# Optimization experiments

Hardware: AMD Instinct MI355X
Metric: run time of the kernel (lower is better)

## Reference

```python
import jax, jax.numpy as jnp
import numpy as np

N, C, H, W = 4, 15, 320, 320
FEATS_OUT, KSIZE, PAD, CONV_PAD, K_RBF = 32, 11, 11, 5, 31
VMAX = 1.0


def _fft2c(x):
    # fastMRI-style centered orthonormal 2D FFT on complex array [..., H, W]
    x = jnp.fft.ifftshift(x, axes=(-2, -1))
    x = jnp.fft.fft2(x, axes=(-2, -1), norm='ortho')
    return jnp.fft.fftshift(x, axes=(-2, -1))


def _ifft2c(x):
    x = jnp.fft.ifftshift(x, axes=(-2, -1))
    x = jnp.fft.ifft2(x, axes=(-2, -1), norm='ortho')
    return jnp.fft.fftshift(x, axes=(-2, -1))


def _to_c(x):
    return jax.lax.complex(x[..., 0], x[..., 1])


def _to_r(z):
    return jnp.stack([jnp.real(z), jnp.imag(z)], axis=-1)


def setup_inputs() -> dict:
    key = jax.random.key(0)
    ks = jax.random.split(key, 8)
    u_t = jax.random.normal(ks[0], (N, H, W, 2), dtype=jnp.float32)
    f = jax.random.normal(ks[1], (N, C, H, W, 2), dtype=jnp.float32)
    coil_sens = jax.random.normal(ks[2], (N, C, H, W, 2), dtype=jnp.float32)
    sampling_mask = (jax.random.uniform(ks[3], (N, H, W)) < 0.35).astype(jnp.float32)
    conv_kernel = jax.random.normal(ks[4], (FEATS_OUT, 1, KSIZE, KSIZE, 2), dtype=jnp.float32)
    conv_kernel = conv_kernel / np.sqrt(KSIZE * KSIZE * 2 * 1)
    conv_kernel = conv_kernel - jnp.mean(conv_kernel, axis=(1, 2, 3, 4), keepdims=True)
    x0 = jnp.linspace(-VMAX, VMAX, K_RBF, dtype=jnp.float32)
    w = jnp.broadcast_to((0.04 * x0).reshape(1, 1, 1, 1, K_RBF), (1, FEATS_OUT, 1, 1, K_RBF)).astype(jnp.float32)
    mu = x0
    sigma = jnp.array([2.0 * VMAX / (K_RBF - 1)], dtype=jnp.float32)
    lamb = jnp.array([1.0], dtype=jnp.float32)
    return {'u_t': u_t, 'f': f, 'coil_sens': coil_sens, 'sampling_mask': sampling_mask,
            'conv_kernel': conv_kernel, 'w': w, 'mu': mu, 'sigma': sigma, 'lamb': lamb}


def reference(u_t, f, coil_sens, sampling_mask, conv_kernel, w, mu, sigma, lamb):
    dn = ('NCHW', 'OIHW', 'NCHW')
    feats_out = conv_kernel.shape[0]
    k = conv_kernel.shape[2]

    # --- regularizer: reflect-pad, complex conv pair, RBF activation, transposed conv pair ---
    pad_cfg = ((0, 0), (0, 0), (PAD, PAD), (PAD, PAD))
    ur = jnp.pad(u_t[:, None, :, :, 0], pad_cfg, mode='reflect')  # [N,1,Hp,Wp]
    ui = jnp.pad(u_t[:, None, :, :, 1], pad_cfg, mode='reflect')

    def conv(x, Wk):
        return jax.lax.conv_general_dilated(x, Wk, (1, 1), [(CONV_PAD, CONV_PAD)] * 2,
                                            dimension_numbers=dn)

    u_k = conv(ur, conv_kernel[..., 0]) + conv(ui, conv_kernel[..., 1])  # [N,Co,Hp,Wp]

    # RBF activation: sum_i w_i * exp(-(x - mu_i)^2 / (2 sigma^2)), scanned over centers
    wk = jnp.transpose(w[0, :, 0, 0, :])  # [K, Co]
    inv2s2 = 1.0 / (2.0 * sigma[0] ** 2)

    def body(acc, wm):
        wi, mi = wm
        acc = acc + wi[None, :, None, None] * jnp.exp(-jnp.square(u_k - mi) * inv2s2)
        return acc, None

    f_u_k, _ = jax.lax.scan(body, jnp.zeros_like(u_k), (wk, mu))

    # conv_transpose2d(padding=CONV_PAD) == conv with flipped kernel, swapped channels, padding k-1-CONV_PAD
    tpad = k - 1 - CONV_PAD

    def convT(x, Wk):
        Wt = jnp.transpose(Wk[:, :, ::-1, ::-1], (1, 0, 2, 3))  # [I,O,k,k] -> OIHW w/ O=1
        return jax.lax.conv_general_dilated(x, Wt, (1, 1), [(tpad, tpad)] * 2,
                                            dimension_numbers=dn)

    Ru_r = convT(f_u_k, conv_kernel[..., 0])[:, 0]  # [N,Hp,Wp]
    Ru_i = convT(f_u_k, conv_kernel[..., 1])[:, 0]
    Ru = jnp.stack([Ru_r, Ru_i], axis=-1)[:, PAD:-PAD, PAD:-PAD, :] / feats_out  # [N,H,W,2]

    # --- data consistency: A^T (A u - f) (cartesian, os=False) ---
    u_c = _to_c(u_t)              # [N,H,W]
    c_c = _to_c(coil_sens)        # [N,C,H,W]
    f_c = _to_c(f)                # [N,C,H,W]
    m = sampling_mask[:, None]    # [N,1,H,W]
    Au = m * _fft2c(u_c[:, None] * c_c)
    At = jnp.sum(_ifft2c(m * (Au - f_c)) * jnp.conj(c_c), axis=1)  # [N,H,W]
    Du = _to_r(At) * lamb[0]

    return u_t - Ru - Du
```

## Files before the change

kernel.cpp:

```cpp
#include <hip/hip_runtime.h>
#include <hip/hip_bf16.h>
#include <math.h>

#define NN 4
#define CC 15
#define HH 320
#define WW 320
#define HW (HH*WW)
#define FF 32
#define KS 11
#define PADN 11
#define CPAD 5
#define HP 342
#define NK 31
#define NCB (NN*CC)
#define TABN 256

typedef short bf16x8 __attribute__((ext_vector_type(8)));
typedef float f32x4 __attribute__((ext_vector_type(4)));
typedef unsigned short u16x4 __attribute__((ext_vector_type(4)));

#define MFMA16 __builtin_amdgcn_mfma_f32_16x16x32_bf16

__device__ __forceinline__ unsigned int pack_bf(float r, float i) {
  __hip_bfloat16 hr = __float2bfloat16(r), hi = __float2bfloat16(i);
  unsigned short ur = *(unsigned short*)&hr, ui = *(unsigned short*)&hi;
  return (unsigned int)ur | ((unsigned int)ui << 16);
}
__device__ __forceinline__ unsigned short f2b(float x) {
  __hip_bfloat16 h = __float2bfloat16(x);
  return *(unsigned short*)&h;
}
__device__ __forceinline__ float b2f(unsigned short u) {
  __hip_bfloat16 h = *(__hip_bfloat16*)&u;
  return __bfloat162float(h);
}
__device__ __forceinline__ unsigned int rot16(unsigned int x) {
  return (x >> 16) | (x << 16);
}

__global__ void k_dft(unsigned int* __restrict__ Fbf) {
  int idx = blockIdx.x * blockDim.x + threadIdx.x;
  if (idx >= HW) return;
  int k = idx / WW, n = idx % WW;
  int prod = (k - 160) * (n - 160);
  int r = prod % 320; if (r < 0) r += 320;
  float ang = -6.283185307179586f * (float)r / 320.0f;
  const float s = 0.05590169943749474f;
  Fbf[idx] = pack_bf(cosf(ang) * s, sinf(ang) * s);
}

__global__ void k_prep(const float* __restrict__ ck, unsigned int* __restrict__ Wpk) {
  int idx = blockIdx.x * blockDim.x + threadIdx.x;
  if (idx >= 32 * 176) return;
  int o = idx / 176, kw = idx % 176;
  int ky = kw / 16, kx = kw % 16;
  unsigned int v = 0;
  if (kx <= 10) {
    const float* p = &ck[(o * 121 + ky * 11 + kx) * 2];
    v = pack_bf(p[0], p[1]);
  }
  Wpk[idx] = v;
}

__global__ void k_prep2(const float* __restrict__ ck, unsigned short* __restrict__ Wt) {
  int idx = blockIdx.x * blockDim.x + threadIdx.x;
  if (idx >= 2 * 11 * 16 * 32) return;
  int o = idx & 31;
  int ky = (idx >> 5) & 15;
  int rest = idx >> 9;
  int kx = rest % 11, ch = rest / 11;
  unsigned short v = 0;
  if (ky <= 10) v = f2b(ck[(o * 121 + ky * 11 + kx) * 2 + ch]);
  Wt[idx] = v;
}

__global__ void k_rbftab(const float* __restrict__ w, const float* __restrict__ mu,
                         const float* __restrict__ sigma, unsigned short* __restrict__ Tab) {
  int o = blockIdx.x;
  int e = threadIdx.x;
  if (e >= TABN + 1) return;
  float v = -2.0f + (float)e * (4.0f / (float)TABN);
  float sg = sigma[0];
  float nInv = -1.0f / (2.0f * sg * sg);
  float acc = 0.f;
  for (int i = 0; i < NK; i++) {
    float d = v - mu[i];
    acc += w[o * NK + i] * __expf(d * d * nInv);
  }
  Tab[o * 260 + e] = f2b(acc);
}

__global__ __launch_bounds__(256) void k_conv_rbf_mfma(
    const float* __restrict__ u_t, const unsigned int* __restrict__ Wpk,
    const unsigned short* __restrict__ Tab, unsigned short* __restrict__ fukT) {
  __shared__ unsigned int lW[32 * 180];
  __shared__ unsigned int tIn[26 * 32];
  __shared__ unsigned short tab[32 * 260];
  int n = blockIdx.z;
  int y0 = blockIdx.y * 16, x0 = blockIdx.x * 16;
  int tid = threadIdx.x;
  for (int i = tid; i < 32 * 176; i += 256)
    lW[(i / 176) * 180 + (i % 176)] = Wpk[i];
  {
    const unsigned int* Ts = (const unsigned int*)Tab;
    unsigned int* Td = (unsigned int*)tab;
    for (int i = tid; i < 32 * 130; i += 256) Td[i] = Ts[i];
  }
  for (int i = tid; i < 26 * 32; i += 256) {
    int rr = i >> 5, cc = i & 31;
    unsigned int v = 0;
    if (cc < 26) {
      int py = y0 + rr - 5, px = x0 + cc - 5;
      if (py >= 0 && py < HP && px >= 0 && px < HP) {
        int uy = py - PADN; uy = uy < 0 ? -uy : (uy >= HH ? 2 * (HH - 1) - uy : uy);
        int ux = px - PADN; ux = ux < 0 ? -ux : (ux >= WW ? 2 * (WW - 1) - ux : ux);
        const float* up = &u_t[((n * HH + uy) * WW + ux) * 2];
        v = pack_bf(up[0], up[1]);
      }
    }
    tIn[i] = v;
  }
  __syncthreads();
  int lane = tid & 63, wave = tid >> 6;
  int m16 = lane & 15, kq = lane >> 4;
  const short* lWs = (const short*)lW;
  f32x4 acc[4][2] = {};
  for (int ky = 0; ky < 11; ky++) {
    bf16x8 af0 = *(const bf16x8*)&lWs[m16 * 360 + ky * 32 + kq * 8];
    bf16x8 af1 = *(const bf16x8*)&lWs[(m16 + 16) * 360 + ky * 32 + kq * 8];
    #pragma unroll
    for (int nt = 0; nt < 4; nt++) {
      int rr = wave * 4 + nt + ky;
      int c0 = rr * 32 + m16 + kq * 4;
      union { unsigned int u[4]; bf16x8 v; } bu;
      bu.u[0] = tIn[c0]; bu.u[1] = tIn[c0 + 1];
      bu.u[2] = tIn[c0 + 2]; bu.u[3] = tIn[c0 + 3];
      acc[nt][0] = MFMA16(af0, bu.v, acc[nt][0], 0, 0, 0);
      acc[nt][1] = MFMA16(af1, bu.v, acc[nt][1], 0, 0, 0);
    }
  }
  const float tscale = (float)TABN / 4.0f;
  #pragma unroll
  for (int nt = 0; nt < 4; nt++) {
    int Y = y0 + wave * 4 + nt;
    int X = x0 + m16;
    if (Y >= HP || X >= HP) continue;
    #pragma unroll
    for (int mt = 0; mt < 2; mt++) {
      u16x4 pk;
      #pragma unroll
      for (int r = 0; r < 4; r++) {
        float v = acc[nt][mt][r];
        int o = mt * 16 + kq * 4 + r;
        float t = (v + 2.0f) * tscale;
        t = fminf(fmaxf(t, 0.0f), 255.999f);
        int i0 = (int)t;
        float fr = t - (float)i0;
        float a = b2f(tab[o * 260 + i0]);
        float bv = b2f(tab[o * 260 + i0 + 1]);
        pk[r] = f2b(a + (bv - a) * fr);
      }
      *(u16x4*)&fukT[(((size_t)n * HP + Y) * HP + X) * 32 + mt * 16 + kq * 4] = pk;
    }
  }
}

__global__ __launch_bounds__(256) void k_convT_mfma(
    const unsigned short* __restrict__ fukT, const unsigned short* __restrict__ Wt,
    float* __restrict__ Ru) {
  __shared__ unsigned short rowBuf[42 * 32];
  __shared__ float accS[16 * 67];
  int n = blockIdx.z;
  int y0 = blockIdx.y * 16, x0 = blockIdx.x * 32;
  int tid = threadIdx.x;
  int lane = tid & 63, wave = tid >> 6;
  int ch = wave >> 1, xh = wave & 1;
  int m16 = lane & 15, kq = lane >> 4;
  bf16x8 afr[11];
  #pragma unroll
  for (int kx = 0; kx < 11; kx++)
    afr[kx] = *(const bf16x8*)&Wt[((ch * 11 + kx) * 16 + m16) * 32 + kq * 8];
  for (int i = tid; i < 16 * 67; i += 256) accS[i] = 0.f;
  int xl = xh * 16 + m16;
  for (int t = 0; t < 26; t++) {
    int r = y0 + 6 + t;
    __syncthreads();
    {
      const unsigned int* src = (const unsigned int*)&fukT[(((size_t)n * HP + r) * HP + x0 + 6) * 32];
      unsigned int* dst = (unsigned int*)rowBuf;
      for (int i = tid; i < 42 * 16; i += 256) dst[i] = src[i];
    }
    __syncthreads();
    f32x4 dacc = {};
    #pragma unroll
    for (int kx = 0; kx < 11; kx++) {
      bf16x8 bfrag = *(const bf16x8*)&rowBuf[(xl + 10 - kx) * 32 + kq * 8];
      dacc = MFMA16(afr[kx], bfrag, dacc, 0, 0, 0);
    }
    #pragma unroll
    for (int rg = 0; rg < 4; rg++) {
      int ky = kq * 4 + rg;
      int y = t + ky - 10;
      if (ky <= 10 && y >= 0 && y < 16)
        accS[y * 67 + xl * 2 + ch] += dacc[rg];
    }
  }
  __syncthreads();
  int chO = tid & 1, xO = (tid >> 1) & 31, yb = tid >> 6;
  #pragma unroll
  for (int q = 0; q < 4; q++) {
    int y = yb + q * 4;
    Ru[(((size_t)n * HH + y0 + y) * WW + x0 + xO) * 2 + chO] = accS[y * 67 + xO * 2 + chO];
  }
}

__global__ void k_umul(const float* __restrict__ u_t, const float* __restrict__ cs,
                       unsigned int* __restrict__ X0) {
  int idx = blockIdx.x * blockDim.x + threadIdx.x;
  if (idx >= NCB * HW) return;
  int hw = idx % HW;
  int n = (idx / HW) / CC;
  float ur = u_t[(n * HW + hw) * 2], ui = u_t[(n * HW + hw) * 2 + 1];
  float cr = cs[idx * 2], ci = cs[idx * 2 + 1];
  X0[idx] = pack_bf(ur * cr - ui * ci, ur * ci + ui * cr);
}

__global__ __launch_bounds__(256) void k_gemm(
    const unsigned int* __restrict__ Abase, long aStride,
    unsigned int xorA1, unsigned int xorA2,
    const unsigned int* __restrict__ Bbase, long bStride, unsigned int xorB,
    unsigned int* __restrict__ OutB, int mode,
    const float* __restrict__ mask, const float* __restrict__ fdat) {
  __shared__ unsigned int lA[64 * 36];
  __shared__ unsigned int lB[32 * 68];
  int b = blockIdx.z;
  int i0 = blockIdx.y * 64, j0 = blockIdx.x * 64;
  const unsigned int* A = Abase + (size_t)b * aStride;
  const unsigned int* B = Bbase + (size_t)b * bStride;
  int tid = threadIdx.x;
  int lane = tid & 63, wave = tid >> 6;
  int wy = (wave >> 1) * 32, wx = (wave & 1) * 32;
  int m16 = lane & 15, kq = lane >> 4;
  f32x4 accR[2][2] = {}, accI[2][2] = {};
  int ar = tid >> 3;
  int ag = tid & 7;
  int bkc = tid >> 4;
  int bc = (tid & 15) * 4;
  uint4 pa0, pa1, pb0, pb1;
  pa0 = *(const uint4*)&A[(i0 + ar) * WW + ag * 4];
  pa1 = *(const uint4*)&A[(i0 + ar + 32) * WW + ag * 4];
  pb0 = *(const uint4*)&B[bkc * WW + j0 + bc];
  pb1 = *(const uint4*)&B[(bkc + 16) * WW + j0 + bc];
  for (int it = 0; it < 10; it++) {
    __syncthreads();
    *(uint4*)&lA[ar * 36 + ag * 4] = pa0;
    *(uint4*)&lA[(ar + 32) * 36 + ag * 4] = pa1;
    *(uint4*)&lB[bkc * 68 + bc] = pb0;
    *(uint4*)&lB[(bkc + 16) * 68 + bc] = pb1;
    __syncthreads();
    if (it < 9) {
      int kc0 = (it + 1) * 32;
      pa0 = *(const uint4*)&A[(i0 + ar) * WW + kc0 + ag * 4];
      pa1 = *(const uint4*)&A[(i0 + ar + 32) * WW + kc0 + ag * 4];
      pb0 = *(const uint4*)&B[(kc0 + bkc) * WW + j0 + bc];
      pb1 = *(const uint4*)&B[(kc0 + bkc + 16) * WW + j0 + bc];
    }
    #pragma unroll
    for (int s = 0; s < 2; s++) {
      bf16x8 a1[2], a2[2], bb[2];
      #pragma unroll
      for (int d = 0; d < 2; d++) {
        int row = wy + d * 16 + m16;
        uint4 p = *(const uint4*)&lA[row * 36 + s * 16 + kq * 4];
        union { unsigned int u[4]; bf16x8 v; } ua, ur2, ub;
        ua.u[0] = p.x ^ xorA1; ua.u[1] = p.y ^ xorA1;
        ua.u[2] = p.z ^ xorA1; ua.u[3] = p.w ^ xorA1;
        a1[d] = ua.v;
        ur2.u[0] = rot16(p.x) ^ xorA2; ur2.u[1] = rot16(p.y) ^ xorA2;
        ur2.u[2] = rot16(p.z) ^ xorA2; ur2.u[3] = rot16(p.w) ^ xorA2;
        a2[d] = ur2.v;
        int col = wx + d * 16 + m16;
        #pragma unroll
        for (int j2 = 0; j2 < 4; j2++)
          ub.u[j2] = lB[(s * 16 + kq * 4 + j2) * 68 + col] ^ xorB;
        bb[d] = ub.v;
      }
      #pragma unroll
      for (int di = 0; di < 2; di++)
        #pragma unroll
        for (int dj = 0; dj < 2; dj++) {
          accR[di][dj] = MFMA16(a1[di], bb[dj], accR[di][dj], 0, 0, 0);
          accI[di][dj] = MFMA16(a2[di], bb[dj], accI[di][dj], 0, 0, 0);
        }
    }
  }
  int n = b / CC;
  #pragma unroll
  for (int di = 0; di < 2; di++)
    #pragma unroll
    for (int dj = 0; dj < 2; dj++)
      #pragma unroll
      for (int r = 0; r < 4; r++) {
        int row = i0 + wy + di * 16 + kq * 4 + r;
        int col = j0 + wx + dj * 16 + m16;
        float vr = accR[di][dj][r], vi = accI[di][dj][r];
        size_t idx = (size_t)b * HW + row * WW + col;
        if (mode == 1) {
          float m = mask[n * HW + row * WW + col];
          vr = m * (vr - fdat[idx * 2]);
          vi = m * (vi - fdat[idx * 2 + 1]);
        }
        OutB[idx] = pack_bf(vr, vi);
      }
}

__global__ void k_coilsum(const unsigned int* __restrict__ Z, const float* __restrict__ cs,
                          float* __restrict__ At) {
  int idx = blockIdx.x * blockDim.x + threadIdx.x;
  if (idx >= NN * HW) return;
  int n = idx / HW, hw = idx % HW;
  float ar = 0.f, ai = 0.f;
  for (int c = 0; c < CC; c++) {
    size_t zi = (size_t)(n * CC + c) * HW + hw;
    unsigned int p = Z[zi];
    float zr = b2f((unsigned short)(p & 0xffff));
    float zim = b2f((unsigned short)(p >> 16));
    float crr = cs[zi * 2], cii = cs[zi * 2 + 1];
    ar += zr * crr + zim * cii;
    ai += zim * crr - zr * cii;
  }
  At[idx * 2] = ar;
  At[idx * 2 + 1] = ai;
}

__global__ void k_final(const float* __restrict__ u_t, const float* __restrict__ Ru,
                        const float* __restrict__ At, const float* __restrict__ lamb,
                        float* __restrict__ out) {
  int idx = blockIdx.x * blockDim.x + threadIdx.x;
  if (idx >= NN * HW * 2) return;
  out[idx] = u_t[idx] - Ru[idx] * (1.0f / (float)FF) - lamb[0] * At[idx];
}

extern "C" void kernel_launch(void* const* d_in, const int* in_sizes, int n_in,
                              void* d_out, int out_size, void* d_ws, size_t ws_size,
                              hipStream_t stream) {
  const float* u_t   = (const float*)d_in[0];
  const float* fdat  = (const float*)d_in[1];
  const float* cs    = (const float*)d_in[2];
  const float* mask  = (const float*)d_in[3];
  const float* ck    = (const float*)d_in[4];
  const float* w     = (const float*)d_in[5];
  const float* mu    = (const float*)d_in[6];
  const float* sigma = (const float*)d_in[7];
  const float* lamb  = (const float*)d_in[8];
  float* out = (float*)d_out;

  unsigned int* wsw = (unsigned int*)d_ws;
  unsigned int* Fbf = wsw;
  unsigned int* Wpk = wsw + 102400;
  unsigned short* Wt = (unsigned short*)(wsw + 108160);
  unsigned short* Tab = (unsigned short*)(wsw + 113792);
  float* At = (float*)(wsw + 117952);
  float* Ru = (float*)(wsw + 937152);
  unsigned int* big = wsw + 1756352;
  unsigned short* fukT = (unsigned short*)big;
  unsigned int* P = big;
  unsigned int* Q = big + 6144000;

  k_dft<<<(HW + 255) / 256, 256, 0, stream>>>(Fbf);
  k_prep<<<(32 * 176 + 255) / 256, 256, 0, stream>>>(ck, Wpk);
  k_prep2<<<(2 * 11 * 16 * 32 + 255) / 256, 256, 0, stream>>>(ck, Wt);
  k_rbftab<<<32, 320, 0, stream>>>(w, mu, sigma, Tab);
  k_conv_rbf_mfma<<<dim3(22, 22, NN), 256, 0, stream>>>(u_t, Wpk, Tab, fukT);
  k_convT_mfma<<<dim3(10, 20, NN), 256, 0, stream>>>(fukT, Wt, Ru);
  k_umul<<<(NCB * HW + 255) / 256, 256, 0, stream>>>(u_t, cs, P);
  k_gemm<<<dim3(5, 5, NCB), 256, 0, stream>>>(Fbf, 0L, 0x80000000u, 0u,
                                              P, (long)HW, 0u,
                                              Q, 0, nullptr, nullptr);
  k_gemm<<<dim3(5, 5, NCB), 256, 0, stream>>>(Q, (long)HW, 0x80000000u, 0u,
                                              Fbf, 0L, 0u,
                                              P, 1, mask, fdat);
  k_gemm<<<dim3(5, 5, NCB), 256, 0, stream>>>(Fbf, 0L, 0u, 0x00008000u,
                                              P, (long)HW, 0u,
                                              Q, 0, nullptr, nullptr);
  k_gemm<<<dim3(5, 5, NCB), 256, 0, stream>>>(Q, (long)HW, 0x80000000u, 0u,
                                              Fbf, 0L, 0x80000000u,
                                              P, 0, nullptr, nullptr);
  k_coilsum<<<(NN * HW + 255) / 256, 256, 0, stream>>>(P, cs, At);
  k_final<<<(NN * HW * 2 + 255) / 256, 256, 0, stream>>>(u_t, Ru, At, lamb, out);
}
```

Before: 379.8 us.

## Fuse paired DFT GEMMs into strip-wise kernels with transposed inputs

Replaces the four separate 64x64-tiled DFT GEMM launches with two kernels, each computing both row and column DFT passes for a 32-row strip while keeping the intermediate in shared memory. The coil-multiply kernel now writes a transposed bf16 layout so both passes can read K-contiguous operands. The mask and k-space subtraction is fused into the first pair, whose output is written transposed. This removes two global round-trips of the large intermediate and two launches, at the cost of large shared memory use, 512-thread blocks and more complex indexing.

```diff
diff --git a/kernel.cpp b/kernel.cpp
--- a/kernel.cpp
+++ b/kernel.cpp
@@ -37,6 +37,17 @@
 }
 __device__ __forceinline__ unsigned int rot16(unsigned int x) {
   return (x >> 16) | (x << 16);
+}
+__device__ __forceinline__ bf16x8 xf4(uint4 p, unsigned int x) {
+  union { unsigned int u[4]; bf16x8 v; } t;
+  t.u[0] = p.x ^ x; t.u[1] = p.y ^ x; t.u[2] = p.z ^ x; t.u[3] = p.w ^ x;
+  return t.v;
+}
+__device__ __forceinline__ bf16x8 xr4(uint4 p, unsigned int x) {
+  union { unsigned int u[4]; bf16x8 v; } t;
+  t.u[0] = rot16(p.x) ^ x; t.u[1] = rot16(p.y) ^ x;
+  t.u[2] = rot16(p.z) ^ x; t.u[3] = rot16(p.w) ^ x;
+  return t.v;
 }
 
 __global__ void k_dft(unsigned int* __restrict__ Fbf) {
@@ -215,104 +226,151 @@
   }
 }
 
-__global__ void k_umul(const float* __restrict__ u_t, const float* __restrict__ cs,
-                       unsigned int* __restrict__ X0) {
-  int idx = blockIdx.x * blockDim.x + threadIdx.x;
-  if (idx >= NCB * HW) return;
-  int hw = idx % HW;
-  int n = (idx / HW) / CC;
-  float ur = u_t[(n * HW + hw) * 2], ui = u_t[(n * HW + hw) * 2 + 1];
-  float cr = cs[idx * 2], ci = cs[idx * 2 + 1];
-  X0[idx] = pack_bf(ur * cr - ui * ci, ur * ci + ui * cr);
-}
-
-__global__ __launch_bounds__(256) void k_gemm(
-    const unsigned int* __restrict__ Abase, long aStride,
-    unsigned int xorA1, unsigned int xorA2,
-    const unsigned int* __restrict__ Bbase, long bStride, unsigned int xorB,
-    unsigned int* __restrict__ OutB, int mode,
-    const float* __restrict__ mask, const float* __restrict__ fdat) {
-  __shared__ unsigned int lA[64 * 36];
-  __shared__ unsigned int lB[32 * 68];
-  int b = blockIdx.z;
-  int i0 = blockIdx.y * 64, j0 = blockIdx.x * 64;
-  const unsigned int* A = Abase + (size_t)b * aStride;
-  const unsigned int* B = Bbase + (size_t)b * bStride;
+__global__ __launch_bounds__(256) void k_umulT(const float* __restrict__ u_t,
+                                               const float* __restrict__ cs,
+                                               unsigned int* __restrict__ X0T) {
+  __shared__ unsigned int t[32 * 33];
+  int bc = blockIdx.x;
+  int b = blockIdx.y;
+  int n = b / CC;
+  int ty = (bc / 10) * 32, tx = (bc % 10) * 32;
+  int r = threadIdx.x >> 5, c = threadIdx.x & 31;
+  #pragma unroll
+  for (int q = 0; q < 4; q++) {
+    int y = ty + r + q * 8, x = tx + c;
+    const float* up = &u_t[((size_t)n * HW + (size_t)y * WW + x) * 2];
+    const float* cp = &cs[((size_t)b * HW + (size_t)y * WW + x) * 2];
+    float ur = up[0], ui = up[1], crr = cp[0], cii = cp[1];
+    t[(r + q * 8) * 33 + c] = pack_bf(ur * crr - ui * cii, ur * cii + ui * crr);
+  }
+  __syncthreads();
+  #pragma unroll
+  for (int q = 0; q < 4; q++) {
+    int xx = r + q * 8;
+    X0T[(size_t)b * HW + (size_t)(tx + xx) * WW + ty + c] = t[c * 33 + xx];
+  }
+}
+
+#define LDB(kc, i) (*(const uint4*)&Bb[(size_t)((i) >> 2) * WW + (kc) * 16 + ((i) & 3) * 4])
+
+template <int MODE>
+__global__ __launch_bounds__(512, 4) void k_dcpair(
+    const unsigned int* __restrict__ Fbf,
+    const unsigned int* __restrict__ Bin,
+    const float* __restrict__ mask, const float* __restrict__ fdat,
+    unsigned int* __restrict__ Out) {
+  __shared__ unsigned int sMem[12800];
+  int bid = blockIdx.x;
+  int wg = (bid & 7) * 75 + (bid >> 3);
+  int b = wg / 10, strip = wg % 10;
+  int i0 = strip * 32;
   int tid = threadIdx.x;
   int lane = tid & 63, wave = tid >> 6;
-  int wy = (wave >> 1) * 32, wx = (wave & 1) * 32;
+  int wr = wave >> 2, wc = wave & 3;
   int m16 = lane & 15, kq = lane >> 4;
-  f32x4 accR[2][2] = {}, accI[2][2] = {};
-  int ar = tid >> 3;
-  int ag = tid & 7;
-  int bkc = tid >> 4;
-  int bc = (tid & 15) * 4;
-  uint4 pa0, pa1, pb0, pb1;
-  pa0 = *(const uint4*)&A[(i0 + ar) * WW + ag * 4];
-  pa1 = *(const uint4*)&A[(i0 + ar + 32) * WW + ag * 4];
-  pb0 = *(const uint4*)&B[bkc * WW + j0 + bc];
-  pb1 = *(const uint4*)&B[(bkc + 16) * WW + j0 + bc];
-  for (int it = 0; it < 10; it++) {
-    __syncthreads();
-    *(uint4*)&lA[ar * 36 + ag * 4] = pa0;
-    *(uint4*)&lA[(ar + 32) * 36 + ag * 4] = pa1;
-    *(uint4*)&lB[bkc * 68 + bc] = pb0;
-    *(uint4*)&lB[(bkc + 16) * 68 + bc] = pb1;
-    __syncthreads();
-    if (it < 9) {
-      int kc0 = (it + 1) * 32;
-      pa0 = *(const uint4*)&A[(i0 + ar) * WW + kc0 + ag * 4];
-      pa1 = *(const uint4*)&A[(i0 + ar + 32) * WW + kc0 + ag * 4];
-      pb0 = *(const uint4*)&B[(kc0 + bkc) * WW + j0 + bc];
-      pb1 = *(const uint4*)&B[(kc0 + bkc + 16) * WW + j0 + bc];
-    }
-    #pragma unroll
-    for (int s = 0; s < 2; s++) {
-      bf16x8 a1[2], a2[2], bb[2];
+  int colBase = wc * 80;
+  const unsigned int XA1 = (MODE == 1) ? 0x80000000u : 0u;
+  const unsigned int XA2 = (MODE == 1) ? 0u : 0x00008000u;
+  const unsigned int* Bb = Bin + (size_t)b * HW;
+  const unsigned int* Arow = Fbf + (size_t)(i0 + wr * 16 + m16) * WW;
+
+  f32x4 aR[5] = {}, aI[5] = {};
+  uint4 p0, p1, p2;
+  p0 = LDB(0, tid); p1 = LDB(0, tid + 512);
+  if (tid < 256) p2 = LDB(0, tid + 1024);
+  uint4 ap = *(const uint4*)&Arow[kq * 4];
+  #pragma unroll
+  for (int kc = 0; kc < 20; kc++) {
+    unsigned int* buf = &sMem[(kc & 1) * 6400];
+    __syncthreads();
+    *(uint4*)&buf[(tid >> 2) * 20 + (tid & 3) * 4] = p0;
+    { int i = tid + 512; *(uint4*)&buf[(i >> 2) * 20 + (i & 3) * 4] = p1; }
+    if (tid < 256) { int i = tid + 1024; *(uint4*)&buf[(i >> 2) * 20 + (i & 3) * 4] = p2; }
+    __syncthreads();
+    bf16x8 a1 = xf4(ap, XA1), a2 = xr4(ap, XA2);
+    if (kc < 19) {
+      p0 = LDB(kc + 1, tid); p1 = LDB(kc + 1, tid + 512);
+      if (tid < 256) p2 = LDB(kc + 1, tid + 1024);
+      ap = *(const uint4*)&Arow[(kc + 1) * 16 + kq * 4];
+    }
+    #pragma unroll
+    for (int ct = 0; ct < 5; ct++) {
+      bf16x8 bb = *(const bf16x8*)&buf[(colBase + ct * 16 + m16) * 20 + kq * 4];
+      aR[ct] = MFMA16(a1, bb, aR[ct], 0, 0, 0);
+      aI[ct] = MFMA16(a2, bb, aI[ct], 0, 0, 0);
+    }
+  }
+  __syncthreads();
+  #pragma unroll
+  for (int ct = 0; ct < 5; ct++)
+    #pragma unroll
+    for (int r = 0; r < 4; r++) {
+      int trow = wr * 16 + kq * 4 + r;
+      int tcol = colBase + ct * 16 + m16;
+      sMem[trow * 324 + tcol] = pack_bf(aR[ct][r], aI[ct][r]);
+    }
+  __syncthreads();
+
+  f32x4 cR[5] = {}, cI[5] = {};
+  int tArow = (wr * 16 + m16) * 324;
+  const unsigned int* Fc[5];
+  uint4 fp[5];
+  #pragma unroll
+  for (int ct = 0; ct < 5; ct++) {
+    Fc[ct] = Fbf + (size_t)(colBase + ct * 16 + m16) * WW;
+    fp[ct] = *(const uint4*)&Fc[ct][kq * 4];
+  }
+  uint4 tp = *(const uint4*)&sMem[tArow + kq * 4];
+  #pragma unroll
+  for (int kc = 0; kc < 20; kc++) {
+    bf16x8 a1 = xf4(tp, 0x80000000u), a2 = xr4(tp, 0u);
+    bf16x8 bcur[5];
+    #pragma unroll
+    for (int ct = 0; ct < 5; ct++)
+      bcur[ct] = (MODE == 2) ? xf4(fp[ct], 0x80000000u) : *(const bf16x8*)&fp[ct];
+    if (kc < 19) {
+      tp = *(const uint4*)&sMem[tArow + (kc + 1) * 16 + kq * 4];
       #pragma unroll
-      for (int d = 0; d < 2; d++) {
-        int row = wy + d * 16 + m16;
-        uint4 p = *(const uint4*)&lA[row * 36 + s * 16 + kq * 4];
-        union { unsigned int u[4]; bf16x8 v; } ua, ur2, ub;
-        ua.u[0] = p.x ^ xorA1; ua.u[1] = p.y ^ xorA1;
-        ua.u[2] = p.z ^ xorA1; ua.u[3] = p.w ^ xorA1;
-        a1[d] = ua.v;
-        ur2.u[0] = rot16(p.x) ^ xorA2; ur2.u[1] = rot16(p.y) ^ xorA2;
-        ur2.u[2] = rot16(p.z) ^ xorA2; ur2.u[3] = rot16(p.w) ^ xorA2;
-        a2[d] = ur2.v;
-        int col = wx + d * 16 + m16;
-        #pragma unroll
-        for (int j2 = 0; j2 < 4; j2++)
-          ub.u[j2] = lB[(s * 16 + kq * 4 + j2) * 68 + col] ^ xorB;
-        bb[d] = ub.v;
-      }
-      #pragma unroll
-      for (int di = 0; di < 2; di++)
-        #pragma unroll
-        for (int dj = 0; dj < 2; dj++) {
-          accR[di][dj] = MFMA16(a1[di], bb[dj], accR[di][dj], 0, 0, 0);
-          accI[di][dj] = MFMA16(a2[di], bb[dj], accI[di][dj], 0, 0, 0);
-        }
-    }
-  }
-  int n = b / CC;
-  #pragma unroll
-  for (int di = 0; di < 2; di++)
-    #pragma unroll
-    for (int dj = 0; dj < 2; dj++)
+      for (int ct = 0; ct < 5; ct++)
+        fp[ct] = *(const uint4*)&Fc[ct][(kc + 1) * 16 + kq * 4];
+    }
+    #pragma unroll
+    for (int ct = 0; ct < 5; ct++) {
+      cR[ct] = MFMA16(a1, bcur[ct], cR[ct], 0, 0, 0);
+      cI[ct] = MFMA16(a2, bcur[ct], cI[ct], 0, 0, 0);
+    }
+  }
+
+  if constexpr (MODE == 1) {
+    __syncthreads();
+    int n = b / CC;
+    #pragma unroll
+    for (int ct = 0; ct < 5; ct++)
       #pragma unroll
       for (int r = 0; r < 4; r++) {
-        int row = i0 + wy + di * 16 + kq * 4 + r;
-        int col = j0 + wx + dj * 16 + m16;
-        float vr = accR[di][dj][r], vi = accI[di][dj][r];
-        size_t idx = (size_t)b * HW + row * WW + col;
-        if (mode == 1) {
-          float m = mask[n * HW + row * WW + col];
-          vr = m * (vr - fdat[idx * 2]);
-          vi = m * (vi - fdat[idx * 2 + 1]);
-        }
-        OutB[idx] = pack_bf(vr, vi);
+        int row = i0 + wr * 16 + kq * 4 + r;
+        int col = colBase + ct * 16 + m16;
+        float m = mask[n * HW + row * WW + col];
+        size_t fi = ((size_t)b * HW + (size_t)row * WW + col) * 2;
+        float vr = m * (cR[ct][r] - fdat[fi]);
+        float vi = m * (cI[ct][r] - fdat[fi + 1]);
+        sMem[col * 33 + (row - i0)] = pack_bf(vr, vi);
       }
+    __syncthreads();
+    for (int i2 = tid; i2 < 320 * 32; i2 += 512) {
+      int x = i2 >> 5, y = i2 & 31;
+      Out[(size_t)b * HW + (size_t)x * WW + i0 + y] = sMem[x * 33 + y];
+    }
+  } else {
+    #pragma unroll
+    for (int ct = 0; ct < 5; ct++)
+      #pragma unroll
+      for (int r = 0; r < 4; r++) {
+        int row = i0 + wr * 16 + kq * 4 + r;
+        int col = colBase + ct * 16 + m16;
+        Out[(size_t)b * HW + (size_t)row * WW + col] = pack_bf(cR[ct][r], cI[ct][r]);
+      }
+  }
 }
 
 __global__ void k_coilsum(const unsigned int* __restrict__ Z, const float* __restrict__ cs,
@@ -365,8 +423,9 @@
   float* Ru = (float*)(wsw + 937152);
   unsigned int* big = wsw + 1756352;
   unsigned short* fukT = (unsigned short*)big;
-  unsigned int* P = big;
-  unsigned int* Q = big + 6144000;
+  unsigned int* X0T = big;
+  unsigned int* P2T = big + 6144000;
+  unsigned int* Q = big;
 
   k_dft<<<(HW + 255) / 256, 256, 0, stream>>>(Fbf);
   k_prep<<<(32 * 176 + 255) / 256, 256, 0, stream>>>(ck, Wpk);
@@ -374,19 +433,9 @@
   k_rbftab<<<32, 320, 0, stream>>>(w, mu, sigma, Tab);
   k_conv_rbf_mfma<<<dim3(22, 22, NN), 256, 0, stream>>>(u_t, Wpk, Tab, fukT);
   k_convT_mfma<<<dim3(10, 20, NN), 256, 0, stream>>>(fukT, Wt, Ru);
-  k_umul<<<(NCB * HW + 255) / 256, 256, 0, stream>>>(u_t, cs, P);
-  k_gemm<<<dim3(5, 5, NCB), 256, 0, stream>>>(Fbf, 0L, 0x80000000u, 0u,
-                                              P, (long)HW, 0u,
-                                              Q, 0, nullptr, nullptr);
-  k_gemm<<<dim3(5, 5, NCB), 256, 0, stream>>>(Q, (long)HW, 0x80000000u, 0u,
-                                              Fbf, 0L, 0u,
-                                              P, 1, mask, fdat);
-  k_gemm<<<dim3(5, 5, NCB), 256, 0, stream>>>(Fbf, 0L, 0u, 0x00008000u,
-                                              P, (long)HW, 0u,
-                                              Q, 0, nullptr, nullptr);
-  k_gemm<<<dim3(5, 5, NCB), 256, 0, stream>>>(Q, (long)HW, 0x80000000u, 0u,
-                                              Fbf, 0L, 0x80000000u,
-                                              P, 0, nullptr, nullptr);
-  k_coilsum<<<(NN * HW + 255) / 256, 256, 0, stream>>>(P, cs, At);
+  k_umulT<<<dim3(100, 60), 256, 0, stream>>>(u_t, cs, X0T);
+  k_dcpair<1><<<600, 512, 0, stream>>>(Fbf, X0T, mask, fdat, P2T);
+  k_dcpair<2><<<600, 512, 0, stream>>>(Fbf, P2T, nullptr, nullptr, Q);
+  k_coilsum<<<(NN * HW + 255) / 256, 256, 0, stream>>>(Q, cs, At);
   k_final<<<(NN * HW * 2 + 255) / 256, 256, 0, stream>>>(u_t, Ru, At, lamb, out);
 }
```

New measurement: 458.5 us. 1.21x slower.
